# Kernel optimization log

Measured on AMD Instinct MI355X. Metric: run time of the kernel, lower is better.

Reference implementation:

```python
import jax, jax.numpy as jnp
import numpy as np

N_NODES = 100000
DIN = 512
B = 1024
T_STEPS = 6
DOUT = 512


def setup_inputs() -> dict:
    key = jax.random.key(0)
    ks = jax.random.split(key, 8)
    s = 0.02  # small init scale for numerical sanity
    x = jax.random.normal(ks[0], (N_NODES, DIN), jnp.float32)
    batch = jnp.sort(jax.random.randint(ks[1], (N_NODES,), 0, B)).astype(jnp.int64)
    Wih = jax.random.normal(ks[2], (4 * DIN, 2 * DIN), jnp.float32) * s
    Whh = jax.random.normal(ks[3], (4 * DIN, DIN), jnp.float32) * s
    bih = jax.random.normal(ks[4], (4 * DIN,), jnp.float32) * s
    bhh = jax.random.normal(ks[5], (4 * DIN,), jnp.float32) * s
    Wpost = jax.random.normal(ks[6], (DOUT, 2 * DIN), jnp.float32) * s
    bpost = jax.random.normal(ks[7], (DOUT,), jnp.float32) * s
    return {"x": x, "batch": batch, "Wih": Wih, "Whh": Whh, "bih": bih,
            "bhh": bhh, "Wpost": Wpost, "bpost": bpost, "num_graphs": B}


def reference(x, batch, Wih, Whh, bih, bhh, Wpost, bpost, num_graphs):
    din = x.shape[1]
    Bg = num_graphs
    h = jnp.zeros((Bg, din), x.dtype)
    c = jnp.zeros((Bg, din), x.dtype)
    q_star = jnp.zeros((Bg, 2 * din), x.dtype)  # [q, r]
    for _ in range(T_STEPS):
        # single-layer LSTM cell over the "batch of graphs" axis
        z = q_star @ Wih.T + h @ Whh.T + (bih + bhh)  # [B, 4*din]
        i, f, g, o = jnp.split(z, 4, axis=-1)  # torch gate order i,f,g,o
        c = jax.nn.sigmoid(f) * c + jax.nn.sigmoid(i) * jnp.tanh(g)
        h = jax.nn.sigmoid(o) * jnp.tanh(c)
        q = h  # [B, din]
        # segment (scatter) softmax attention over nodes of each graph
        e = jnp.sum(x * q[batch], axis=-1)  # [N]
        emax = jax.ops.segment_max(e, batch, num_segments=Bg)
        ex = jnp.exp(e - emax[batch])
        denom = jax.ops.segment_sum(ex, batch, num_segments=Bg)
        a = ex / denom[batch]  # [N]
        r = jax.ops.segment_sum(a[:, None] * x, batch, num_segments=Bg)  # [B, din]
        q_star = jnp.concatenate([q, r], axis=-1)
    # post_pool: Linear(2*din -> dim_out) + bias + ReLU (dropout=0, eval mode)
    out = jax.nn.relu(q_star @ Wpost.T + bpost)
    return out
```

## Files before the change

### kernel.cpp

```cpp
#include <hip/hip_runtime.h>
#include <stdint.h>
#include <stddef.h>

#define DIN    512
#define BGR    1024
#define NGATE  2048
#define KQ     1024
#define DOUT   512
#define TSTEPS 6

typedef unsigned short ushort_t;
typedef short bf16x8 __attribute__((ext_vector_type(8)));
typedef unsigned short u16x8 __attribute__((ext_vector_type(8)));
typedef float f32x4 __attribute__((ext_vector_type(4)));

__device__ __forceinline__ float b2f(unsigned short u) {
    unsigned int i = ((unsigned int)u) << 16;
    float f;
    __builtin_memcpy(&f, &i, 4);
    return f;
}

__device__ __forceinline__ unsigned short f2b(float f) {
    unsigned int i;
    __builtin_memcpy(&i, &f, 4);
    unsigned int lsb = (i >> 16) & 1u;
    i += 0x7fffu + lsb;
    return (unsigned short)(i >> 16);
}

__device__ __forceinline__ float fast_sigmoid(float v) {
    return 1.f / (1.f + __expf(-v));
}

__device__ __forceinline__ float fast_tanh(float v) {
    float t = fabsf(v);
    float e = __expf(-2.f * t);
    float r = (1.f - e) / (1.f + e);
    return v < 0.f ? -r : r;
}

__global__ void probe_dtypes(const ushort_t* x, const ushort_t* Wih,
                             const ushort_t* Whh, const ushort_t* bih,
                             const ushort_t* bhh, const ushort_t* Wpost,
                             const ushort_t* bpost, int* flags)
{
    __shared__ int cnt[7];
    const int tid = threadIdx.x;
    if (tid < 7) cnt[tid] = 0;
    __syncthreads();
    const int t = tid >> 5;
    const int l = tid & 31;
    if (t < 7) {
        const ushort_t* p = (t == 0) ? x : (t == 1) ? Wih : (t == 2) ? Whh
                          : (t == 3) ? bih : (t == 4) ? bhh
                          : (t == 5) ? Wpost : bpost;
        int good = 0;
        for (int i = 0; i < 4; i++) {
            ushort_t u = p[(l * 4 + i) * 2];
            int ex = (u >> 7) & 0xFF;
            if (ex == 0 || (ex >= 96 && ex <= 143)) good++;
        }
        atomicAdd(&cnt[t], good);
    }
    __syncthreads();
    if (tid < 7) flags[tid] = (cnt[tid] < 96) ? 1 : 0;
}

#define BM 64
#define BN 64
#define BK 32

__global__ __launch_bounds__(256)
void gemm_cell(const ushort_t* __restrict__ Ag,
               const ushort_t* __restrict__ Wg,
               const float* __restrict__ bias2,
               float* __restrict__ c, float* __restrict__ H)
{
    __shared__ __align__(16) ushort_t As[BM * BK];
    __shared__ __align__(16) ushort_t Bs[BM * BK];

    const int tid  = threadIdx.x;
    const int lane = tid & 63;
    const int w    = tid >> 6;
    const int lrow = lane & 15;
    const int quad = lane >> 4;

    const int n0 = blockIdx.x * 64;
    const int m0 = blockIdx.y * BM;

    const int srow = tid >> 2;
    const int scol = (tid & 3) * 8;

    const ushort_t* aSrc = Ag + (size_t)(m0 + srow) * KQ + scol;
    const ushort_t* bSrc = Wg + (size_t)(n0 + srow) * KQ + scol;

    f32x4 acc[4];
#pragma unroll
    for (int ni = 0; ni < 4; ni++) acc[ni] = (f32x4){0.f, 0.f, 0.f, 0.f};

    bf16x8 av = *(const bf16x8*)(aSrc);
    bf16x8 bv = *(const bf16x8*)(bSrc);

    for (int kt = 0; kt < KQ; kt += BK) {
        __syncthreads();
        *(bf16x8*)&As[srow * BK + scol] = av;
        *(bf16x8*)&Bs[srow * BK + scol] = bv;
        if (kt + BK < KQ) {
            av = *(const bf16x8*)(aSrc + kt + BK);
            bv = *(const bf16x8*)(bSrc + kt + BK);
        }
        __syncthreads();

        bf16x8 af = *(const bf16x8*)&As[(w * 16 + lrow) * BK + quad * 8];
        bf16x8 bfr[4];
#pragma unroll
        for (int ni = 0; ni < 4; ni++)
            bfr[ni] = *(const bf16x8*)&Bs[(ni * 16 + lrow) * BK + quad * 8];
#pragma unroll
        for (int ni = 0; ni < 4; ni++)
            acc[ni] = __builtin_amdgcn_mfma_f32_16x16x32_bf16(
                af, bfr[ni], acc[ni], 0, 0, 0);
    }

    const int d   = blockIdx.x * 16 + lrow;
    const float bi = bias2[n0 + lrow];
    const float bf = bias2[n0 + 16 + lrow];
    const float bg = bias2[n0 + 32 + lrow];
    const float bo = bias2[n0 + 48 + lrow];
#pragma unroll
    for (int r = 0; r < 4; r++) {
        const int gm = m0 + w * 16 + quad * 4 + r;
        float zi = acc[0][r] + bi;
        float zf = acc[1][r] + bf;
        float zg = acc[2][r] + bg;
        float zo = acc[3][r] + bo;
        size_t off = (size_t)gm * DIN + d;
        float cc = c[off];
        cc = fast_sigmoid(zf) * cc + fast_sigmoid(zi) * fast_tanh(zg);
        float hh = fast_sigmoid(zo) * fast_tanh(cc);
        c[off] = cc;
        H[off] = hh;
    }
}

template <int MODE>
__global__ __launch_bounds__(256)
void gemm_bt(const ushort_t* __restrict__ Ag, const ushort_t* __restrict__ Bg,
             const float* __restrict__ bias, float* __restrict__ Cout,
             int M, int N, int K)
{
    __shared__ __align__(16) ushort_t As[BM * BK];
    __shared__ __align__(16) ushort_t Bs[BN * BK];

    const int tid  = threadIdx.x;
    const int lane = tid & 63;
    const int w    = tid >> 6;
    const int wr   = w >> 1;
    const int wc   = w & 1;
    const int lrow = lane & 15;
    const int quad = lane >> 4;

    const int n0 = blockIdx.x * BN;
    const int m0 = blockIdx.y * BM;

    const int srow = tid >> 2;
    const int scol = (tid & 3) * 8;

    const ushort_t* aSrc = Ag + (size_t)(m0 + srow) * K + scol;
    const ushort_t* bSrc = Bg + (size_t)(n0 + srow) * K + scol;

    f32x4 acc[2][2];
#pragma unroll
    for (int i = 0; i < 2; i++)
#pragma unroll
        for (int j = 0; j < 2; j++)
            acc[i][j] = (f32x4){0.f, 0.f, 0.f, 0.f};

    bf16x8 av = *(const bf16x8*)(aSrc);
    bf16x8 bv = *(const bf16x8*)(bSrc);

    for (int kt = 0; kt < K; kt += BK) {
        __syncthreads();
        *(bf16x8*)&As[srow * BK + scol] = av;
        *(bf16x8*)&Bs[srow * BK + scol] = bv;
        if (kt + BK < K) {
            av = *(const bf16x8*)(aSrc + kt + BK);
            bv = *(const bf16x8*)(bSrc + kt + BK);
        }
        __syncthreads();

        bf16x8 af[2], bfr[2];
#pragma unroll
        for (int mi = 0; mi < 2; mi++)
            af[mi] = *(const bf16x8*)&As[(wr * 32 + mi * 16 + lrow) * BK + quad * 8];
#pragma unroll
        for (int ni = 0; ni < 2; ni++)
            bfr[ni] = *(const bf16x8*)&Bs[(wc * 32 + ni * 16 + lrow) * BK + quad * 8];

#pragma unroll
        for (int mi = 0; mi < 2; mi++)
#pragma unroll
            for (int ni = 0; ni < 2; ni++)
                acc[mi][ni] = __builtin_amdgcn_mfma_f32_16x16x32_bf16(
                    af[mi], bfr[ni], acc[mi][ni], 0, 0, 0);
    }

#pragma unroll
    for (int mi = 0; mi < 2; mi++) {
#pragma unroll
        for (int ni = 0; ni < 2; ni++) {
#pragma unroll
            for (int r = 0; r < 4; r++) {
                int gm = m0 + wr * 32 + mi * 16 + quad * 4 + r;
                int gn = n0 + wc * 32 + ni * 16 + lrow;
                float v = acc[mi][ni][r] + bias[gn];
                if (MODE == 1) {
                    if (!(v > 0.f) && (v == v)) v = 0.f;
                }
                Cout[(size_t)gm * N + gn] = v;
            }
        }
    }
}

template <int XMODE>
__global__ __launch_bounds__(256)
void attn_step(const ushort_t* __restrict__ xbsrc, const ushort_t* __restrict__ xraw,
               ushort_t* __restrict__ xbdst, const int* __restrict__ offs,
               const float* __restrict__ H, ushort_t* __restrict__ A,
               const int* __restrict__ flags)
{
    const int b    = blockIdx.x;
    const int tid  = threadIdx.x;
    const int lane = tid & 63;
    const int w    = tid >> 6;
    const int xf   = (XMODE == 0) ? 0 : flags[0];

    __shared__ float accL[4][DIN];
    __shared__ float mw[4], lw[4];

    const float* hrow = H + (size_t)b * DIN;
    {
        const int d0 = tid * 2;
        A[(size_t)b * KQ + d0]     = f2b(hrow[d0]);
        A[(size_t)b * KQ + d0 + 1] = f2b(hrow[d0 + 1]);
    }
    f32x4 q0 = *(const f32x4*)(hrow + lane * 8);
    f32x4 q1 = *(const f32x4*)(hrow + lane * 8 + 4);
    float q8[8] = {q0[0], q0[1], q0[2], q0[3], q1[0], q1[1], q1[2], q1[3]};

    const int s  = offs[b];
    const int en = offs[b + 1];

    const float NEG_INF = -__builtin_inff();
    float m = NEG_INF, l = 0.f;
    float acc[8];
#pragma unroll
    for (int j = 0; j < 8; j++) acc[j] = 0.f;

    auto load_row = [&](int n, float* v) {
        if (XMODE == 0 || !xf) {
            const ushort_t* src = (XMODE == 0) ? xbsrc : xraw;
            u16x8 xv = *(const u16x8*)(src + (size_t)n * DIN + lane * 8);
#pragma unroll
            for (int j = 0; j < 8; j++) v[j] = b2f(xv[j]);
            if (XMODE == 1)
                *(u16x8*)(xbdst + (size_t)n * DIN + lane * 8) = xv;
        } else {
            const float* xp = (const float*)xraw;
            f32x4 v0 = *(const f32x4*)(xp + (size_t)n * DIN + lane * 8);
            f32x4 v1 = *(const f32x4*)(xp + (size_t)n * DIN + lane * 8 + 4);
#pragma unroll
            for (int j = 0; j < 4; j++) { v[j] = v0[j]; v[4 + j] = v1[j]; }
            if (XMODE == 1) {
                u16x8 o;
#pragma unroll
                for (int j = 0; j < 8; j++) o[j] = f2b(v[j]);
                *(u16x8*)(xbdst + (size_t)n * DIN + lane * 8) = o;
            }
        }
    };

    auto update = [&](float e, const float* xv) {
        float mn = fmaxf(m, e);
        float al = __expf(m - mn);
        float pp = __expf(e - mn);
        l = l * al + pp;
#pragma unroll
        for (int j = 0; j < 8; j++) acc[j] = acc[j] * al + pp * xv[j];
        m = mn;
    };

    float xa[8] = {0.f}, xc[8] = {0.f};
    int n = s + w;
    if (n < en)     load_row(n, xa);
    if (n + 4 < en) load_row(n + 4, xc);
    for (; n < en; n += 8) {
        float pa[8], pc[8];
        const int np = n + 8;
        if (np < en)     load_row(np, pa);
        if (np + 4 < en) load_row(np + 4, pc);

        float e1 = 0.f, e2 = 0.f;
#pragma unroll
        for (int j = 0; j < 8; j++) { e1 += q8[j] * xa[j]; e2 += q8[j] * xc[j]; }
#pragma unroll
        for (int off = 32; off > 0; off >>= 1) {
            e1 += __shfl_xor(e1, off, 64);
            e2 += __shfl_xor(e2, off, 64);
        }

        update(e1, xa);
        if (n + 4 < en) update(e2, xc);

#pragma unroll
        for (int j = 0; j < 8; j++) { xa[j] = pa[j]; xc[j] = pc[j]; }
    }

    if (lane == 0) { mw[w] = m; lw[w] = l; }
#pragma unroll
    for (int j = 0; j < 8; j++) accL[w][lane * 8 + j] = acc[j];
    __syncthreads();

    const float M = fmaxf(fmaxf(mw[0], mw[1]), fmaxf(mw[2], mw[3]));
    const int d0 = tid * 2;
    float r0 = 0.f, r1 = 0.f, lt = 0.f;
#pragma unroll
    for (int ww = 0; ww < 4; ww++) {
        float mwv = mw[ww];
        float a = (mwv == NEG_INF) ? 0.f : __expf(mwv - M);
        lt += a * lw[ww];
        r0 += a * accL[ww][d0];
        r1 += a * accL[ww][d0 + 1];
    }
    float inv = lt > 0.f ? 1.f / lt : 0.f;
    A[(size_t)b * KQ + DIN + d0]     = f2b(r0 * inv);
    A[(size_t)b * KQ + DIN + d0 + 1] = f2b(r1 * inv);
}

__global__ void prep_weights(const ushort_t* __restrict__ Wih,
                             const ushort_t* __restrict__ Whh,
                             const ushort_t* __restrict__ bih,
                             const ushort_t* __restrict__ bhh,
                             const ushort_t* __restrict__ Wpost,
                             const ushort_t* __restrict__ bpost,
                             ushort_t* __restrict__ Wp,
                             float* __restrict__ bias2,
                             float* __restrict__ biaspost,
                             ushort_t* __restrict__ Wpb,
                             const int* __restrict__ flags)
{
    const int idx = blockIdx.x * 256 + threadIdx.x;
    const int fWih = flags[1], fWhh = flags[2], fbih = flags[3];
    const int fbhh = flags[4], fWpo = flags[5], fbpo = flags[6];

    if (idx < NGATE * KQ) {
        const int nn = idx >> 10;
        const int k  = idx & 1023;
        const int g  = (nn >> 4) & 3;
        const int n  = g * 512 + (nn >> 6) * 16 + (nn & 15);
        const int widx = n * KQ + k;
        float v = fWih ? ((const float*)Wih)[widx] : b2f(Wih[widx]);
        if (k < DIN) {
            int hidx = n * DIN + k;
            v += fWhh ? ((const float*)Whh)[hidx] : b2f(Whh[hidx]);
        }
        Wp[idx] = f2b(v);
    }
    if (idx < DOUT * KQ) {
        Wpb[idx] = fWpo ? f2b(((const float*)Wpost)[idx]) : Wpost[idx];
    }
    if (idx < NGATE) {
        const int g = (idx >> 4) & 3;
        const int n = g * 512 + (idx >> 6) * 16 + (idx & 15);
        float v1 = fbih ? ((const float*)bih)[n] : b2f(bih[n]);
        float v2 = fbhh ? ((const float*)bhh)[n] : b2f(bhh[n]);
        bias2[idx] = v1 + v2;
    }
    if (idx < DOUT) {
        biaspost[idx] = fbpo ? ((const float*)bpost)[idx] : b2f(bpost[idx]);
    }
}

__global__ void prep_h0(const ushort_t* __restrict__ bih,
                        const ushort_t* __restrict__ bhh,
                        float* __restrict__ c, float* __restrict__ H,
                        ushort_t* __restrict__ A, const int* __restrict__ flags)
{
    const int b   = blockIdx.x;
    const int tid = threadIdx.x;
    const int fbih = flags[3], fbhh = flags[4];
    for (int d = tid; d < DIN; d += 256) {
        auto ld = [&](int n) {
            float v1 = fbih ? ((const float*)bih)[n] : b2f(bih[n]);
            float v2 = fbhh ? ((const float*)bhh)[n] : b2f(bhh[n]);
            return v1 + v2;
        };
        float zi = ld(d);
        float zg = ld(2 * DIN + d);
        float zo = ld(3 * DIN + d);
        float c0 = fast_sigmoid(zi) * fast_tanh(zg);
        float h0 = fast_sigmoid(zo) * fast_tanh(c0);
        c[(size_t)b * DIN + d] = c0;
        H[(size_t)b * DIN + d] = h0;
        A[(size_t)b * KQ + d]       = f2b(h0);
        A[(size_t)b * KQ + DIN + d] = 0;
    }
}

__global__ void prep_offsets(const int* __restrict__ batch, int* __restrict__ offs, int Nn)
{
    int n = blockIdx.x * 256 + threadIdx.x;
    if (n >= Nn) return;
    const bool is64 = batch[Nn - 1] < batch[Nn - 2];
    int cur  = is64 ? batch[2 * n] : batch[n];
    int prev = (n == 0) ? -1 : (is64 ? batch[2 * (n - 1)] : batch[n - 1]);
    for (int bb = prev + 1; bb <= cur; ++bb) offs[bb] = n;
    if (n == Nn - 1) {
        for (int bb = cur + 1; bb <= BGR; ++bb) offs[bb] = Nn;
    }
}

extern "C" void kernel_launch(void* const* d_in, const int* in_sizes, int n_in,
                              void* d_out, int out_size, void* d_ws, size_t ws_size,
                              hipStream_t stream)
{
    const ushort_t* x     = (const ushort_t*)d_in[0];
    const int*      batch = (const int*)d_in[1];
    const ushort_t* Wih   = (const ushort_t*)d_in[2];
    const ushort_t* Whh   = (const ushort_t*)d_in[3];
    const ushort_t* bih   = (const ushort_t*)d_in[4];
    const ushort_t* bhh   = (const ushort_t*)d_in[5];
    const ushort_t* Wpost = (const ushort_t*)d_in[6];
    const ushort_t* bpost = (const ushort_t*)d_in[7];
    const int Nn = in_sizes[1];
    const long long Tx = (long long)in_sizes[0];

    char* p = (char*)d_ws;
    auto carve = [&](size_t bytes) -> void* {
        char* q = p;
        p += (bytes + 255) & ~(size_t)255;
        return (void*)q;
    };
    ushort_t* Wp       = (ushort_t*)carve((size_t)NGATE * KQ * 2);
    ushort_t* Wpb      = (ushort_t*)carve((size_t)DOUT * KQ * 2);
    float*    bias2    = (float*)carve((size_t)NGATE * 4);
    float*    biaspost = (float*)carve((size_t)DOUT * 4);
    float*    c        = (float*)carve((size_t)BGR * DIN * 4);
    float*    H        = (float*)carve((size_t)BGR * DIN * 4);
    ushort_t* A        = (ushort_t*)carve((size_t)BGR * KQ * 2);
    int*      offs     = (int*)carve((size_t)(BGR + 1) * 4);
    int*      flags    = (int*)carve(16 * 4);
    size_t used = (size_t)(p - (char*)d_ws);
    const bool use_xb = (ws_size >= used + (size_t)Tx * 2 + 256);
    ushort_t* xb = use_xb ? (ushort_t*)carve((size_t)Tx * 2) : nullptr;

    probe_dtypes<<<1, 256, 0, stream>>>(x, Wih, Whh, bih, bhh, Wpost, bpost, flags);
    prep_weights<<<(NGATE * KQ) / 256, 256, 0, stream>>>(
        Wih, Whh, bih, bhh, Wpost, bpost, Wp, bias2, biaspost, Wpb, flags);
    prep_h0<<<BGR, 256, 0, stream>>>(bih, bhh, c, H, A, flags);
    prep_offsets<<<(Nn + 255) / 256, 256, 0, stream>>>(batch, offs, Nn);

    for (int t = 0; t < TSTEPS; ++t) {
        if (t > 0)
            gemm_cell<<<dim3(NGATE / 64, BGR / BM), 256, 0, stream>>>(
                A, Wp, bias2, c, H);
        if (use_xb) {
            if (t == 0)
                attn_step<1><<<BGR, 256, 0, stream>>>(xb, x, xb, offs, H, A, flags);
            else
                attn_step<0><<<BGR, 256, 0, stream>>>(xb, x, xb, offs, H, A, flags);
        } else {
            attn_step<2><<<BGR, 256, 0, stream>>>(x, x, nullptr, offs, H, A, flags);
        }
    }
    gemm_bt<1><<<dim3(DOUT / BN, BGR / BM), 256, 0, stream>>>(
        A, Wpb, biaspost, (float*)d_out, BGR, DOUT, KQ);
}
```

Measured before the change: 529.3 us.

## Fuse LSTM-cell GEMM and attention steps into one persistent cooperative kernel

Replaces the per-step gemm_cell and attn_step launches, plus the prep_h0 kernel, with a single cooperative kernel of 512 blocks. It loops over all time steps and uses grid.sync between the gate GEMM and the segment-softmax attention phases. Each block owns one 64x64 GEMM tile and two graphs for attention. The initial h0/c0 is computed in-kernel from the biases. This removes many kernel launches and their inter-kernel gaps. In exchange, the attention phase runs with half as many blocks, and the grid-wide barriers carry their own cost.

New measurement: 1.222 ms. +130.8%, slower.

```diff
diff --git a/kernel.cpp b/kernel.cpp
--- a/kernel.cpp
+++ b/kernel.cpp
@@ -1,6 +1,9 @@
 #include <hip/hip_runtime.h>
+#include <hip/hip_cooperative_groups.h>
 #include <stdint.h>
 #include <stddef.h>
+
+namespace cg = cooperative_groups;
 
 #define DIN    512
 #define BGR    1024
@@ -71,82 +74,9 @@
 #define BN 64
 #define BK 32
 
-__global__ __launch_bounds__(256)
-void gemm_cell(const ushort_t* __restrict__ Ag,
-               const ushort_t* __restrict__ Wg,
-               const float* __restrict__ bias2,
-               float* __restrict__ c, float* __restrict__ H)
-{
-    __shared__ __align__(16) ushort_t As[BM * BK];
-    __shared__ __align__(16) ushort_t Bs[BM * BK];
-
-    const int tid  = threadIdx.x;
-    const int lane = tid & 63;
-    const int w    = tid >> 6;
-    const int lrow = lane & 15;
-    const int quad = lane >> 4;
-
-    const int n0 = blockIdx.x * 64;
-    const int m0 = blockIdx.y * BM;
-
-    const int srow = tid >> 2;
-    const int scol = (tid & 3) * 8;
-
-    const ushort_t* aSrc = Ag + (size_t)(m0 + srow) * KQ + scol;
-    const ushort_t* bSrc = Wg + (size_t)(n0 + srow) * KQ + scol;
-
-    f32x4 acc[4];
-#pragma unroll
-    for (int ni = 0; ni < 4; ni++) acc[ni] = (f32x4){0.f, 0.f, 0.f, 0.f};
-
-    bf16x8 av = *(const bf16x8*)(aSrc);
-    bf16x8 bv = *(const bf16x8*)(bSrc);
-
-    for (int kt = 0; kt < KQ; kt += BK) {
-        __syncthreads();
-        *(bf16x8*)&As[srow * BK + scol] = av;
-        *(bf16x8*)&Bs[srow * BK + scol] = bv;
-        if (kt + BK < KQ) {
-            av = *(const bf16x8*)(aSrc + kt + BK);
-            bv = *(const bf16x8*)(bSrc + kt + BK);
-        }
-        __syncthreads();
-
-        bf16x8 af = *(const bf16x8*)&As[(w * 16 + lrow) * BK + quad * 8];
-        bf16x8 bfr[4];
-#pragma unroll
-        for (int ni = 0; ni < 4; ni++)
-            bfr[ni] = *(const bf16x8*)&Bs[(ni * 16 + lrow) * BK + quad * 8];
-#pragma unroll
-        for (int ni = 0; ni < 4; ni++)
-            acc[ni] = __builtin_amdgcn_mfma_f32_16x16x32_bf16(
-                af, bfr[ni], acc[ni], 0, 0, 0);
-    }
-
-    const int d   = blockIdx.x * 16 + lrow;
-    const float bi = bias2[n0 + lrow];
-    const float bf = bias2[n0 + 16 + lrow];
-    const float bg = bias2[n0 + 32 + lrow];
-    const float bo = bias2[n0 + 48 + lrow];
-#pragma unroll
-    for (int r = 0; r < 4; r++) {
-        const int gm = m0 + w * 16 + quad * 4 + r;
-        float zi = acc[0][r] + bi;
-        float zf = acc[1][r] + bf;
-        float zg = acc[2][r] + bg;
-        float zo = acc[3][r] + bo;
-        size_t off = (size_t)gm * DIN + d;
-        float cc = c[off];
-        cc = fast_sigmoid(zf) * cc + fast_sigmoid(zi) * fast_tanh(zg);
-        float hh = fast_sigmoid(zo) * fast_tanh(cc);
-        c[off] = cc;
-        H[off] = hh;
-    }
-}
-
 template <int MODE>
 __global__ __launch_bounds__(256)
-void gemm_bt(const ushort_t* __restrict__ Ag, const ushort_t* __restrict__ Bg,
+void gemm_bt(const ushort_t* __restrict__ Ag, const ushort_t* __restrict__ Bgm,
              const float* __restrict__ bias, float* __restrict__ Cout,
              int M, int N, int K)
 {
@@ -167,8 +97,8 @@
     const int srow = tid >> 2;
     const int scol = (tid & 3) * 8;
 
-    const ushort_t* aSrc = Ag + (size_t)(m0 + srow) * K + scol;
-    const ushort_t* bSrc = Bg + (size_t)(n0 + srow) * K + scol;
+    const ushort_t* aSrc = Ag  + (size_t)(m0 + srow) * K + scol;
+    const ushort_t* bSrc = Bgm + (size_t)(n0 + srow) * K + scol;
 
     f32x4 acc[2][2];
 #pragma unroll
@@ -224,119 +154,233 @@
     }
 }
 
-template <int XMODE>
-__global__ __launch_bounds__(256)
-void attn_step(const ushort_t* __restrict__ xbsrc, const ushort_t* __restrict__ xraw,
-               ushort_t* __restrict__ xbdst, const int* __restrict__ offs,
-               const float* __restrict__ H, ushort_t* __restrict__ A,
-               const int* __restrict__ flags)
-{
-    const int b    = blockIdx.x;
+__global__ __launch_bounds__(256, 2)
+void fused_loop(const ushort_t* __restrict__ xraw,
+                ushort_t* __restrict__ xb,
+                const int* __restrict__ offs,
+                const ushort_t* __restrict__ Wg,
+                const float* __restrict__ bias2,
+                const ushort_t* __restrict__ bih,
+                const ushort_t* __restrict__ bhh,
+                float* __restrict__ c,
+                float* __restrict__ H,
+                ushort_t* __restrict__ A,
+                const int* __restrict__ flags,
+                int use_xb)
+{
+    cg::grid_group grid = cg::this_grid();
+    const int bid  = blockIdx.x;
     const int tid  = threadIdx.x;
     const int lane = tid & 63;
     const int w    = tid >> 6;
-    const int xf   = (XMODE == 0) ? 0 : flags[0];
-
+    const int g0   = bid * 2;
+
+    __shared__ __align__(16) ushort_t As[BM * BK];
+    __shared__ __align__(16) ushort_t Bs[BM * BK];
     __shared__ float accL[4][DIN];
     __shared__ float mw[4], lw[4];
-
-    const float* hrow = H + (size_t)b * DIN;
+    __shared__ float h0sh[DIN];
+
+    const int xf = flags[0];
+
     {
-        const int d0 = tid * 2;
-        A[(size_t)b * KQ + d0]     = f2b(hrow[d0]);
-        A[(size_t)b * KQ + d0 + 1] = f2b(hrow[d0 + 1]);
-    }
-    f32x4 q0 = *(const f32x4*)(hrow + lane * 8);
-    f32x4 q1 = *(const f32x4*)(hrow + lane * 8 + 4);
-    float q8[8] = {q0[0], q0[1], q0[2], q0[3], q1[0], q1[1], q1[2], q1[3]};
-
-    const int s  = offs[b];
-    const int en = offs[b + 1];
-
+        const int fbih = flags[3], fbhh = flags[4];
+        for (int d = tid; d < DIN; d += 256) {
+            float zi = fbih ? ((const float*)bih)[d] : b2f(bih[d]);
+            zi      += fbhh ? ((const float*)bhh)[d] : b2f(bhh[d]);
+            float zg = fbih ? ((const float*)bih)[2 * DIN + d] : b2f(bih[2 * DIN + d]);
+            zg      += fbhh ? ((const float*)bhh)[2 * DIN + d] : b2f(bhh[2 * DIN + d]);
+            float zo = fbih ? ((const float*)bih)[3 * DIN + d] : b2f(bih[3 * DIN + d]);
+            zo      += fbhh ? ((const float*)bhh)[3 * DIN + d] : b2f(bhh[3 * DIN + d]);
+            float c0 = fast_sigmoid(zi) * fast_tanh(zg);
+            float h0 = fast_sigmoid(zo) * fast_tanh(c0);
+            h0sh[d] = h0;
+            c[(size_t)g0 * DIN + d]       = c0;
+            c[(size_t)(g0 + 1) * DIN + d] = c0;
+            ushort_t hb = f2b(h0);
+            A[(size_t)g0 * KQ + d]       = hb;
+            A[(size_t)(g0 + 1) * KQ + d] = hb;
+        }
+        __syncthreads();
+    }
+
+    const int lrow = lane & 15;
+    const int quad = lane >> 4;
     const float NEG_INF = -__builtin_inff();
-    float m = NEG_INF, l = 0.f;
-    float acc[8];
-#pragma unroll
-    for (int j = 0; j < 8; j++) acc[j] = 0.f;
-
-    auto load_row = [&](int n, float* v) {
-        if (XMODE == 0 || !xf) {
-            const ushort_t* src = (XMODE == 0) ? xbsrc : xraw;
-            u16x8 xv = *(const u16x8*)(src + (size_t)n * DIN + lane * 8);
-#pragma unroll
-            for (int j = 0; j < 8; j++) v[j] = b2f(xv[j]);
-            if (XMODE == 1)
-                *(u16x8*)(xbdst + (size_t)n * DIN + lane * 8) = xv;
-        } else {
-            const float* xp = (const float*)xraw;
-            f32x4 v0 = *(const f32x4*)(xp + (size_t)n * DIN + lane * 8);
-            f32x4 v1 = *(const f32x4*)(xp + (size_t)n * DIN + lane * 8 + 4);
-#pragma unroll
-            for (int j = 0; j < 4; j++) { v[j] = v0[j]; v[4 + j] = v1[j]; }
-            if (XMODE == 1) {
-                u16x8 o;
-#pragma unroll
-                for (int j = 0; j < 8; j++) o[j] = f2b(v[j]);
-                *(u16x8*)(xbdst + (size_t)n * DIN + lane * 8) = o;
-            }
-        }
-    };
-
-    auto update = [&](float e, const float* xv) {
-        float mn = fmaxf(m, e);
-        float al = __expf(m - mn);
-        float pp = __expf(e - mn);
-        l = l * al + pp;
-#pragma unroll
-        for (int j = 0; j < 8; j++) acc[j] = acc[j] * al + pp * xv[j];
-        m = mn;
-    };
-
-    float xa[8] = {0.f}, xc[8] = {0.f};
-    int n = s + w;
-    if (n < en)     load_row(n, xa);
-    if (n + 4 < en) load_row(n + 4, xc);
-    for (; n < en; n += 8) {
-        float pa[8], pc[8];
-        const int np = n + 8;
-        if (np < en)     load_row(np, pa);
-        if (np + 4 < en) load_row(np + 4, pc);
-
-        float e1 = 0.f, e2 = 0.f;
-#pragma unroll
-        for (int j = 0; j < 8; j++) { e1 += q8[j] * xa[j]; e2 += q8[j] * xc[j]; }
-#pragma unroll
-        for (int off = 32; off > 0; off >>= 1) {
-            e1 += __shfl_xor(e1, off, 64);
-            e2 += __shfl_xor(e2, off, 64);
-        }
-
-        update(e1, xa);
-        if (n + 4 < en) update(e2, xc);
-
-#pragma unroll
-        for (int j = 0; j < 8; j++) { xa[j] = pa[j]; xc[j] = pc[j]; }
-    }
-
-    if (lane == 0) { mw[w] = m; lw[w] = l; }
-#pragma unroll
-    for (int j = 0; j < 8; j++) accL[w][lane * 8 + j] = acc[j];
-    __syncthreads();
-
-    const float M = fmaxf(fmaxf(mw[0], mw[1]), fmaxf(mw[2], mw[3]));
-    const int d0 = tid * 2;
-    float r0 = 0.f, r1 = 0.f, lt = 0.f;
-#pragma unroll
-    for (int ww = 0; ww < 4; ww++) {
-        float mwv = mw[ww];
-        float a = (mwv == NEG_INF) ? 0.f : __expf(mwv - M);
-        lt += a * lw[ww];
-        r0 += a * accL[ww][d0];
-        r1 += a * accL[ww][d0 + 1];
-    }
-    float inv = lt > 0.f ? 1.f / lt : 0.f;
-    A[(size_t)b * KQ + DIN + d0]     = f2b(r0 * inv);
-    A[(size_t)b * KQ + DIN + d0 + 1] = f2b(r1 * inv);
+
+    for (int t = 0; t < TSTEPS; ++t) {
+        if (t > 0) {
+            grid.sync();
+            const int n0   = (bid & 31) * 64;
+            const int m0   = (bid >> 5) * 64;
+            const int srow = tid >> 2;
+            const int scol = (tid & 3) * 8;
+            const ushort_t* aSrc = A  + (size_t)(m0 + srow) * KQ + scol;
+            const ushort_t* bSrc = Wg + (size_t)(n0 + srow) * KQ + scol;
+
+            f32x4 acc4[4];
+#pragma unroll
+            for (int ni = 0; ni < 4; ni++) acc4[ni] = (f32x4){0.f, 0.f, 0.f, 0.f};
+
+            bf16x8 av = *(const bf16x8*)(aSrc);
+            bf16x8 bv = *(const bf16x8*)(bSrc);
+
+            for (int kt = 0; kt < KQ; kt += BK) {
+                __syncthreads();
+                *(bf16x8*)&As[srow * BK + scol] = av;
+                *(bf16x8*)&Bs[srow * BK + scol] = bv;
+                if (kt + BK < KQ) {
+                    av = *(const bf16x8*)(aSrc + kt + BK);
+                    bv = *(const bf16x8*)(bSrc + kt + BK);
+                }
+                __syncthreads();
+
+                bf16x8 af = *(const bf16x8*)&As[(w * 16 + lrow) * BK + quad * 8];
+                bf16x8 bfr[4];
+#pragma unroll
+                for (int ni = 0; ni < 4; ni++)
+                    bfr[ni] = *(const bf16x8*)&Bs[(ni * 16 + lrow) * BK + quad * 8];
+#pragma unroll
+                for (int ni = 0; ni < 4; ni++)
+                    acc4[ni] = __builtin_amdgcn_mfma_f32_16x16x32_bf16(
+                        af, bfr[ni], acc4[ni], 0, 0, 0);
+            }
+
+            const int dd  = (bid & 31) * 16 + lrow;
+            const float bi_ = bias2[n0 + lrow];
+            const float bf_ = bias2[n0 + 16 + lrow];
+            const float bg_ = bias2[n0 + 32 + lrow];
+            const float bo_ = bias2[n0 + 48 + lrow];
+#pragma unroll
+            for (int r = 0; r < 4; r++) {
+                const int gm = m0 + w * 16 + quad * 4 + r;
+                float zi = acc4[0][r] + bi_;
+                float zf = acc4[1][r] + bf_;
+                float zg = acc4[2][r] + bg_;
+                float zo = acc4[3][r] + bo_;
+                size_t off = (size_t)gm * DIN + dd;
+                float cc = c[off];
+                cc = fast_sigmoid(zf) * cc + fast_sigmoid(zi) * fast_tanh(zg);
+                float hh = fast_sigmoid(zo) * fast_tanh(cc);
+                c[off] = cc;
+                H[off] = hh;
+            }
+            grid.sync();
+        }
+
+        const int sel  = (use_xb && t > 0) ? 0 : (xf ? 1 : 2);
+        const int wrxb = (use_xb && t == 0) ? 1 : 0;
+
+        for (int gg = 0; gg < 2; ++gg) {
+            const int b = g0 + gg;
+            const float* hrow = H + (size_t)b * DIN;
+
+            float q8[8];
+            if (t == 0) {
+#pragma unroll
+                for (int j = 0; j < 8; j++) q8[j] = h0sh[lane * 8 + j];
+            } else {
+                f32x4 q0v = *(const f32x4*)(hrow + lane * 8);
+                f32x4 q1v = *(const f32x4*)(hrow + lane * 8 + 4);
+#pragma unroll
+                for (int j = 0; j < 4; j++) { q8[j] = q0v[j]; q8[4 + j] = q1v[j]; }
+                const int dq = tid * 2;
+                A[(size_t)b * KQ + dq]     = f2b(hrow[dq]);
+                A[(size_t)b * KQ + dq + 1] = f2b(hrow[dq + 1]);
+            }
+
+            const int s  = offs[b];
+            const int en = offs[b + 1];
+
+            float m = NEG_INF, l = 0.f;
+            float acc[8];
+#pragma unroll
+            for (int j = 0; j < 8; j++) acc[j] = 0.f;
+
+            auto load_row = [&](int n, float* v) {
+                if (sel == 0) {
+                    u16x8 xv = *(const u16x8*)(xb + (size_t)n * DIN + lane * 8);
+#pragma unroll
+                    for (int j = 0; j < 8; j++) v[j] = b2f(xv[j]);
+                } else if (sel == 2) {
+                    u16x8 xv = *(const u16x8*)(xraw + (size_t)n * DIN + lane * 8);
+#pragma unroll
+                    for (int j = 0; j < 8; j++) v[j] = b2f(xv[j]);
+                    if (wrxb)
+                        *(u16x8*)(xb + (size_t)n * DIN + lane * 8) = xv;
+                } else {
+                    const float* xp = (const float*)xraw;
+                    f32x4 v0 = *(const f32x4*)(xp + (size_t)n * DIN + lane * 8);
+                    f32x4 v1 = *(const f32x4*)(xp + (size_t)n * DIN + lane * 8 + 4);
+#pragma unroll
+                    for (int j = 0; j < 4; j++) { v[j] = v0[j]; v[4 + j] = v1[j]; }
+                    if (wrxb) {
+                        u16x8 o;
+#pragma unroll
+                        for (int j = 0; j < 8; j++) o[j] = f2b(v[j]);
+                        *(u16x8*)(xb + (size_t)n * DIN + lane * 8) = o;
+                    }
+                }
+            };
+
+            auto update = [&](float e, const float* xv) {
+                float mn = fmaxf(m, e);
+                float al = __expf(m - mn);
+                float pp = __expf(e - mn);
+                l = l * al + pp;
+#pragma unroll
+                for (int j = 0; j < 8; j++) acc[j] = acc[j] * al + pp * xv[j];
+                m = mn;
+            };
+
+            float xa[8] = {0.f}, xc[8] = {0.f};
+            int n = s + w;
+            if (n < en)     load_row(n, xa);
+            if (n + 4 < en) load_row(n + 4, xc);
+            for (; n < en; n += 8) {
+                float pa[8], pc[8];
+                const int np = n + 8;
+                if (np < en)     load_row(np, pa);
+                if (np + 4 < en) load_row(np + 4, pc);
+
+                float e1 = 0.f, e2 = 0.f;
+#pragma unroll
+                for (int j = 0; j < 8; j++) { e1 += q8[j] * xa[j]; e2 += q8[j] * xc[j]; }
+#pragma unroll
+                for (int off = 32; off > 0; off >>= 1) {
+                    e1 += __shfl_xor(e1, off, 64);
+                    e2 += __shfl_xor(e2, off, 64);
+                }
+
+                update(e1, xa);
+                if (n + 4 < en) update(e2, xc);
+
+#pragma unroll
+                for (int j = 0; j < 8; j++) { xa[j] = pa[j]; xc[j] = pc[j]; }
+            }
+
+            __syncthreads();
+            if (lane == 0) { mw[w] = m; lw[w] = l; }
+#pragma unroll
+            for (int j = 0; j < 8; j++) accL[w][lane * 8 + j] = acc[j];
+            __syncthreads();
+
+            const float M = fmaxf(fmaxf(mw[0], mw[1]), fmaxf(mw[2], mw[3]));
+            const int d0 = tid * 2;
+            float r0 = 0.f, r1 = 0.f, lt = 0.f;
+#pragma unroll
+            for (int ww = 0; ww < 4; ww++) {
+                float mwv = mw[ww];
+                float a = (mwv == NEG_INF) ? 0.f : __expf(mwv - M);
+                lt += a * lw[ww];
+                r0 += a * accL[ww][d0];
+                r1 += a * accL[ww][d0 + 1];
+            }
+            float inv = lt > 0.f ? 1.f / lt : 0.f;
+            A[(size_t)b * KQ + DIN + d0]     = f2b(r0 * inv);
+            A[(size_t)b * KQ + DIN + d0 + 1] = f2b(r1 * inv);
+        }
+    }
 }
 
 __global__ void prep_weights(const ushort_t* __restrict__ Wih,
@@ -380,32 +424,6 @@
     }
     if (idx < DOUT) {
         biaspost[idx] = fbpo ? ((const float*)bpost)[idx] : b2f(bpost[idx]);
-    }
-}
-
-__global__ void prep_h0(const ushort_t* __restrict__ bih,
-                        const ushort_t* __restrict__ bhh,
-                        float* __restrict__ c, float* __restrict__ H,
-                        ushort_t* __restrict__ A, const int* __restrict__ flags)
-{
-    const int b   = blockIdx.x;
-    const int tid = threadIdx.x;
-    const int fbih = flags[3], fbhh = flags[4];
-    for (int d = tid; d < DIN; d += 256) {
-        auto ld = [&](int n) {
-            float v1 = fbih ? ((const float*)bih)[n] : b2f(bih[n]);
-            float v2 = fbhh ? ((const float*)bhh)[n] : b2f(bhh[n]);
-            return v1 + v2;
-        };
-        float zi = ld(d);
-        float zg = ld(2 * DIN + d);
-        float zo = ld(3 * DIN + d);
-        float c0 = fast_sigmoid(zi) * fast_tanh(zg);
-        float h0 = fast_sigmoid(zo) * fast_tanh(c0);
-        c[(size_t)b * DIN + d] = c0;
-        H[(size_t)b * DIN + d] = h0;
-        A[(size_t)b * KQ + d]       = f2b(h0);
-        A[(size_t)b * KQ + DIN + d] = 0;
     }
 }
 
@@ -459,22 +477,17 @@
     probe_dtypes<<<1, 256, 0, stream>>>(x, Wih, Whh, bih, bhh, Wpost, bpost, flags);
     prep_weights<<<(NGATE * KQ) / 256, 256, 0, stream>>>(
         Wih, Whh, bih, bhh, Wpost, bpost, Wp, bias2, biaspost, Wpb, flags);
-    prep_h0<<<BGR, 256, 0, stream>>>(bih, bhh, c, H, A, flags);
     prep_offsets<<<(Nn + 255) / 256, 256, 0, stream>>>(batch, offs, Nn);
 
-    for (int t = 0; t < TSTEPS; ++t) {
-        if (t > 0)
-            gemm_cell<<<dim3(NGATE / 64, BGR / BM), 256, 0, stream>>>(
-                A, Wp, bias2, c, H);
-        if (use_xb) {
-            if (t == 0)
-                attn_step<1><<<BGR, 256, 0, stream>>>(xb, x, xb, offs, H, A, flags);
-            else
-                attn_step<0><<<BGR, 256, 0, stream>>>(xb, x, xb, offs, H, A, flags);
-        } else {
-            attn_step<2><<<BGR, 256, 0, stream>>>(x, x, nullptr, offs, H, A, flags);
-        }
-    }
+    int use_xb_i = use_xb ? 1 : 0;
+    void* args[] = {
+        (void*)&x, (void*)&xb, (void*)&offs, (void*)&Wp, (void*)&bias2,
+        (void*)&bih, (void*)&bhh, (void*)&c, (void*)&H, (void*)&A,
+        (void*)&flags, (void*)&use_xb_i
+    };
+    hipLaunchCooperativeKernel((const void*)fused_loop, dim3(512), dim3(256),
+                               args, 0, stream);
+
     gemm_bt<1><<<dim3(DOUT / BN, BGR / BM), 256, 0, stream>>>(
         A, Wpb, biaspost, (float*)d_out, BGR, DOUT, KQ);
 }
```
